# Kernel tuning notes

Hardware: AMD Instinct MI355X
Metric: run time of the kernel (lower is better)

## Reference

```python
import jax, jax.numpy as jnp
import numpy as np
from jax import lax

N = 32768      # points in the single input cloud
NIN = 16       # input per-point features
NH = 64        # nhidden
NOUT = 2
K = 32         # max_neighbors
DEPTH = 3
RADII = (2.0, 4.0, 8.0)
DIM = NH + 4   # PPFConv message dim: x_j (NH) + 4 point-pair features
CHUNK = 1024   # query chunk for brute-force radius search


def _fps(pos, n_samples):
    """Farthest point sampling, deterministic start at index 0 (eval mode)."""
    n = pos.shape[0]
    big = jnp.asarray(np.finfo(np.float32).max, pos.dtype)

    def body(carry, _):
        dists, last = carry
        d = jnp.sum((pos - pos[last]) ** 2, axis=-1)
        dists = jnp.minimum(dists, d)
        nxt = jnp.argmax(dists).astype(jnp.int32)
        return (dists, nxt), nxt

    init = (jnp.full((n,), big, pos.dtype), jnp.int32(0))
    _, rest = lax.scan(body, init, None, length=n_samples - 1)
    return jnp.concatenate([jnp.zeros((1,), jnp.int32), rest])


def _radius_knn(pos_q, pos, r, k):
    """For each query: indices of up to k points within radius r (+ validity mask).
    Chunked over queries so the [nq, n] distance matrix is never fully materialized."""
    nq = pos_q.shape[0]

    def f(qc):
        d2 = jnp.sum((qc[:, None, :] - pos[None, :, :]) ** 2, axis=-1)  # [CHUNK, n]
        neg_d2, idx = lax.top_k(-d2, k)
        valid = (-neg_d2) <= r * r
        return idx, valid

    idx, valid = lax.map(f, pos_q.reshape(-1, CHUNK, 3))
    return idx.reshape(nq, k), valid.reshape(nq, k)


def _angle(v1, v2):
    c = jnp.cross(v1, v2)
    return jnp.arctan2(jnp.linalg.norm(c, axis=-1), jnp.sum(v1 * v2, axis=-1))


def _ppf(pos_i, pos_j, n_i, n_j):
    d = pos_j - pos_i
    return jnp.stack([
        jnp.linalg.norm(d, axis=-1),
        _angle(n_i, d),
        _angle(n_j, d),
        _angle(n_i, n_j),
    ], axis=-1)


def _forward(x, pos, norm, lin_in_w0, lin_in_b0, lin_in_w1, lin_in_b1,
             sa_nn1_w0, sa_nn1_b0, sa_nn1_w1, sa_nn1_b1, sa_nn2_w, sa_nn2_b,
             lin_out_w0, lin_out_b0, lin_out_w1, lin_out_b1):
    # lin_in MLP
    h = jax.nn.relu(x @ lin_in_w0 + lin_in_b0)
    h = jax.nn.relu(h @ lin_in_w1 + lin_in_b1)

    cur_x, cur_pos, cur_norm = h, pos, norm
    for i in range(DEPTH):  # SAModules (structurally distinct levels)
        n_samples = cur_pos.shape[0] // 2  # ratio = 0.5
        idx = _fps(cur_pos, n_samples)
        pos_q = cur_pos[idx]
        norm_q = cur_norm[idx]
        nbr, valid = _radius_knn(pos_q, cur_pos, RADII[i], K)  # [nq, K]
        x_j = cur_x[nbr]                                       # [nq, K, NH]
        feats = _ppf(pos_q[:, None, :], cur_pos[nbr], norm_q[:, None, :], cur_norm[nbr])
        msg = jnp.concatenate([x_j, feats], axis=-1)           # [nq, K, DIM]
        # PPFConv local nn (nn1): Linear+ReLU x2
        m = jax.nn.relu(msg @ sa_nn1_w0[i] + sa_nn1_b0[i])
        m = jax.nn.relu(m @ sa_nn1_w1[i] + sa_nn1_b1[i])
        # max aggregation over valid neighbors (empty -> 0, matching torch_scatter)
        m = jnp.where(valid[..., None], m, -1e30)
        agg = jnp.max(m, axis=1)
        agg = jnp.where(valid.any(axis=1)[:, None], agg, 0.0)
        # PPFConv global nn (nn2): Linear+ReLU
        cur_x = jax.nn.relu(agg @ sa_nn2_w[i] + sa_nn2_b[i])
        cur_pos, cur_norm = pos_q, norm_q

    # global_mean_pool over the single graph -> [1, NH]
    pooled = jnp.mean(cur_x, axis=0, keepdims=True)
    o = jax.nn.relu(pooled @ lin_out_w0 + lin_out_b0)
    return o @ lin_out_w1 + lin_out_b1  # [1, NOUT]


_forward_jit = jax.jit(_forward)


def setup_inputs() -> dict:
    key = jax.random.key(0)
    ks = jax.random.split(key, 20)

    def w(k, *shape):
        return jax.random.normal(k, shape, jnp.float32) * float(np.sqrt(2.0 / shape[-2]))

    def b(k, *shape):
        return jax.random.normal(k, shape, jnp.float32) * 0.01

    x = jax.random.normal(ks[0], (N, NIN), jnp.float32)
    pos = jax.random.uniform(ks[1], (N, 3), dtype=jnp.float32) * 32.0  # unit density cube
    nrm = jax.random.normal(ks[2], (N, 3), jnp.float32)
    norm = nrm / jnp.linalg.norm(nrm, axis=-1, keepdims=True)

    return dict(
        x=x, pos=pos, norm=norm,
        lin_in_w0=w(ks[3], NIN, NH), lin_in_b0=b(ks[4], NH),
        lin_in_w1=w(ks[5], NH, NH), lin_in_b1=b(ks[6], NH),
        sa_nn1_w0=w(ks[7], DEPTH, DIM, DIM), sa_nn1_b0=b(ks[8], DEPTH, DIM),
        sa_nn1_w1=w(ks[9], DEPTH, DIM, DIM), sa_nn1_b1=b(ks[10], DEPTH, DIM),
        sa_nn2_w=w(ks[11], DEPTH, DIM, NH), sa_nn2_b=b(ks[12], DEPTH, NH),
        lin_out_w0=w(ks[13], NH, NH), lin_out_b0=b(ks[14], NH),
        lin_out_w1=w(ks[15], NH, NOUT), lin_out_b1=b(ks[16], NOUT),
    )


def reference(x, pos, norm, lin_in_w0, lin_in_b0, lin_in_w1, lin_in_b1,
              sa_nn1_w0, sa_nn1_b0, sa_nn1_w1, sa_nn1_b1, sa_nn2_w, sa_nn2_b,
              lin_out_w0, lin_out_b0, lin_out_w1, lin_out_b1):
    return _forward_jit(x, pos, norm, lin_in_w0, lin_in_b0, lin_in_w1, lin_in_b1,
                        sa_nn1_w0, sa_nn1_b0, sa_nn1_w1, sa_nn1_b1, sa_nn2_w, sa_nn2_b,
                        lin_out_w0, lin_out_b0, lin_out_w1, lin_out_b1)
```

## Files before the change

### kernel.cpp

```cpp
#include <hip/hip_runtime.h>
#include <math.h>

typedef unsigned long long u64;

#define TILE 2048
#define CAP 96
#define QB 32
#define NCELL 4096

__device__ __forceinline__ u64 wave_min_u64(u64 v) {
#pragma unroll
  for (int off = 32; off; off >>= 1) {
    u64 o = __shfl_xor(v, off, 64);
    v = (o < v) ? o : v;
  }
  return v;
}

__device__ __forceinline__ u64 wave_max_u64(u64 v) {
#pragma unroll
  for (int off = 32; off; off >>= 1) {
    u64 o = __shfl_xor(v, off, 64);
    v = (o > v) ? o : v;
  }
  return v;
}

__device__ __forceinline__ float angf(float ax, float ay, float az,
                                      float bx, float by, float bz) {
  float cx = ay * bz - az * by;
  float cy = az * bx - ax * bz;
  float cz = ax * by - ay * bx;
  float cn = sqrtf(cx * cx + cy * cy + cz * cz);
  float dt = ax * bx + ay * by + az * bz;
  return atan2f(cn, dt);
}

__device__ __forceinline__ int cell_of(float x, float y, float z) {
  int cx = (int)(x * 0.5f); cx = cx < 0 ? 0 : (cx > 15 ? 15 : cx);
  int cy = (int)(y * 0.5f); cy = cy < 0 ? 0 : (cy > 15 ? 15 : cy);
  int cz = (int)(z * 0.5f); cz = cz < 0 ? 0 : (cz > 15 ? 15 : cz);
  return (cz << 8) | (cy << 4) | cx;
}

__global__ __launch_bounds__(256) void k_lin_in(
    const float* __restrict__ x, const float* __restrict__ w0,
    const float* __restrict__ b0, const float* __restrict__ w1,
    const float* __restrict__ b1, float* __restrict__ h) {
  __shared__ __align__(16) float sW0[1024];
  __shared__ __align__(16) float sW1[4096];
  __shared__ float sB0[64], sB1[64];
  for (int i = threadIdx.x; i < 1024; i += 256) sW0[i] = w0[i];
  for (int i = threadIdx.x; i < 4096; i += 256) sW1[i] = w1[i];
  if (threadIdx.x < 64) { sB0[threadIdx.x] = b0[threadIdx.x]; sB1[threadIdx.x] = b1[threadIdx.x]; }
  __syncthreads();
  int p = blockIdx.x * 256 + threadIdx.x;
  float h1[64];
#pragma unroll
  for (int o = 0; o < 64; ++o) h1[o] = sB0[o];
#pragma unroll
  for (int c4 = 0; c4 < 4; ++c4) {
    float4 xv = *(const float4*)&x[p * 16 + 4 * c4];
#pragma unroll
    for (int u = 0; u < 4; ++u) {
      float v = (u == 0) ? xv.x : (u == 1) ? xv.y : (u == 2) ? xv.z : xv.w;
      int c = 4 * c4 + u;
#pragma unroll
      for (int o4 = 0; o4 < 16; ++o4) {
        float4 w = *(const float4*)&sW0[c * 64 + 4 * o4];
        h1[4 * o4 + 0] = fmaf(v, w.x, h1[4 * o4 + 0]);
        h1[4 * o4 + 1] = fmaf(v, w.y, h1[4 * o4 + 1]);
        h1[4 * o4 + 2] = fmaf(v, w.z, h1[4 * o4 + 2]);
        h1[4 * o4 + 3] = fmaf(v, w.w, h1[4 * o4 + 3]);
      }
    }
  }
#pragma unroll
  for (int o = 0; o < 64; ++o) h1[o] = fmaxf(h1[o], 0.f);
  float h2[64];
#pragma unroll
  for (int o = 0; o < 64; ++o) h2[o] = sB1[o];
#pragma unroll
  for (int c = 0; c < 64; ++c) {
    float v = h1[c];
#pragma unroll
    for (int o4 = 0; o4 < 16; ++o4) {
      float4 w = *(const float4*)&sW1[c * 64 + 4 * o4];
      h2[4 * o4 + 0] = fmaf(v, w.x, h2[4 * o4 + 0]);
      h2[4 * o4 + 1] = fmaf(v, w.y, h2[4 * o4 + 1]);
      h2[4 * o4 + 2] = fmaf(v, w.z, h2[4 * o4 + 2]);
      h2[4 * o4 + 3] = fmaf(v, w.w, h2[4 * o4 + 3]);
    }
  }
#pragma unroll
  for (int o4 = 0; o4 < 16; ++o4) {
    float4 o;
    o.x = fmaxf(h2[4 * o4 + 0], 0.f);
    o.y = fmaxf(h2[4 * o4 + 1], 0.f);
    o.z = fmaxf(h2[4 * o4 + 2], 0.f);
    o.w = fmaxf(h2[4 * o4 + 3], 0.f);
    *(float4*)&h[(long)p * 64 + 4 * o4] = o;
  }
}

__global__ __launch_bounds__(256) void k_precompA(
    const float* __restrict__ feat, const float* __restrict__ w,
    const float* __restrict__ b, float* __restrict__ A, int n) {
  __shared__ __align__(16) float sW[4352];
  __shared__ float sB[68];
  for (int i = threadIdx.x; i < 4352; i += 256) sW[i] = w[i];
  for (int i = threadIdx.x; i < 68; i += 256) sB[i] = b[i];
  __syncthreads();
  int p = blockIdx.x * 256 + threadIdx.x;
  if (p >= n) return;
  float acc[68];
#pragma unroll
  for (int o = 0; o < 68; ++o) acc[o] = sB[o];
#pragma unroll
  for (int c4 = 0; c4 < 16; ++c4) {
    float4 f = *(const float4*)&feat[(long)p * 64 + 4 * c4];
#pragma unroll
    for (int u = 0; u < 4; ++u) {
      float v = (u == 0) ? f.x : (u == 1) ? f.y : (u == 2) ? f.z : f.w;
      int c = 4 * c4 + u;
#pragma unroll
      for (int o4 = 0; o4 < 17; ++o4) {
        float4 wv = *(const float4*)&sW[c * 68 + 4 * o4];
        acc[4 * o4 + 0] = fmaf(v, wv.x, acc[4 * o4 + 0]);
        acc[4 * o4 + 1] = fmaf(v, wv.y, acc[4 * o4 + 1]);
        acc[4 * o4 + 2] = fmaf(v, wv.z, acc[4 * o4 + 2]);
        acc[4 * o4 + 3] = fmaf(v, wv.w, acc[4 * o4 + 3]);
      }
    }
  }
#pragma unroll
  for (int o4 = 0; o4 < 17; ++o4) {
    float4 o;
    o.x = acc[4 * o4 + 0]; o.y = acc[4 * o4 + 1];
    o.z = acc[4 * o4 + 2]; o.w = acc[4 * o4 + 3];
    *(float4*)&A[(long)p * 68 + 4 * o4] = o;
  }
}

__global__ __launch_bounds__(256) void k_zero_counts(int* __restrict__ c) {
  int i = blockIdx.x * 256 + threadIdx.x;
  if (i < NCELL) c[i] = 0;
}

__global__ __launch_bounds__(256) void k_hist(const float* __restrict__ pos,
                                              int n, int* __restrict__ counts) {
  int i = blockIdx.x * 256 + threadIdx.x;
  if (i >= n) return;
  atomicAdd(&counts[cell_of(pos[3 * i], pos[3 * i + 1], pos[3 * i + 2])], 1);
}

__global__ __launch_bounds__(512) void k_scan(const int* __restrict__ counts,
                                              int* __restrict__ starts,
                                              int* __restrict__ offs) {
  __shared__ int ps[512];
  int t = threadIdx.x;
  int loc[8], s = 0;
#pragma unroll
  for (int k = 0; k < 8; ++k) { loc[k] = counts[t * 8 + k]; s += loc[k]; }
  ps[t] = s;
  __syncthreads();
  for (int off = 1; off < 512; off <<= 1) {
    int v = (t >= off) ? ps[t - off] : 0;
    __syncthreads();
    ps[t] += v;
    __syncthreads();
  }
  int run = ps[t] - s;
#pragma unroll
  for (int k = 0; k < 8; ++k) {
    starts[t * 8 + k] = run;
    offs[t * 8 + k] = run;
    run += loc[k];
  }
  if (t == 511) starts[NCELL] = run;
}

__global__ __launch_bounds__(256) void k_scatter(
    const float* __restrict__ pos, int n, int* __restrict__ offs,
    float4* __restrict__ pts, int* __restrict__ sid, int* __restrict__ slot0) {
  int i = blockIdx.x * 256 + threadIdx.x;
  if (i >= n) return;
  float x = pos[3 * i], y = pos[3 * i + 1], z = pos[3 * i + 2];
  int c = cell_of(x, y, z);
  int slot = atomicAdd(&offs[c], 1);
  pts[slot] = make_float4(x, y, z, 3.402823466e38f);
  sid[slot] = i;
  if (i == 0) *slot0 = slot;
}

__global__ __launch_bounds__(512) void k_fps_cell(
    float4* __restrict__ pts, const int* __restrict__ sid,
    const int* __restrict__ starts, const int* __restrict__ slot0, int m,
    int* __restrict__ sel) {
#pragma clang fp contract(off)
  __shared__ u64 ck[NCELL];
  __shared__ int cs[NCELL + 1];
  __shared__ unsigned short sl[NCELL];
  __shared__ float bx[NCELL], by[NCELL], bz[NCELL];
  __shared__ int scnt[2];
  __shared__ u64 wk[2][8];
  const int t = threadIdx.x, lane = t & 63, wv = t >> 6;
  const u64 lmask = (1ull << lane) - 1ull;
  const unsigned* ckhi = (const unsigned*)ck;
  for (int c = t; c < NCELL + 1; c += 512) cs[c] = starts[c];
  __syncthreads();
  for (int c = t; c < NCELL; c += 512)
    ck[c] = (cs[c + 1] > cs[c]) ? ((u64)0x7F7FFFFFu << 32) : 0ull;
  if (t < 2) scnt[t] = 0;
  if (t == 0) sel[0] = 0;
  __syncthreads();
  float4 cp = pts[*slot0];
  float px = cp.x, py = cp.y, pz = cp.z;
  for (int i = 1; i < m; ++i) {
    const int par = i & 1;
    bool sv[8];
#pragma unroll
    for (int k = 0; k < 8; ++k) {
      int c = t + 512 * k;
      unsigned drmax = ckhi[2 * c + 1];
      float cx = (float)(((c & 15) << 1) + 1);
      float cy = (float)((((c >> 4) & 15) << 1) + 1);
      float cz = (float)(((c >> 8) << 1) + 1);
      float dx = fmaxf(fabsf(px - cx) - 1.f, 0.f);
      float dy = fmaxf(fabsf(py - cy) - 1.f, 0.f);
      float dz = fmaxf(fabsf(pz - cz) - 1.f, 0.f);
      float mind2 = (dx * dx + dy * dy) + dz * dz;
      sv[k] = __float_as_uint(mind2 * 0.9999f) < drmax;
    }
    u64 msk[8];
    int wtot = 0;
#pragma unroll
    for (int k = 0; k < 8; ++k) {
      msk[k] = __ballot(sv[k]);
      wtot += __popcll(msk[k]);
    }
    int wbase = 0;
    if (lane == 0 && wtot) wbase = atomicAdd(&scnt[par], wtot);
    wbase = __shfl(wbase, 0, 64);
#pragma unroll
    for (int k = 0; k < 8; ++k) {
      if (sv[k])
        sl[wbase + __popcll(msk[k] & lmask)] = (unsigned short)(t + 512 * k);
      wbase += __popcll(msk[k]);
    }
    if (t == 0) scnt[par ^ 1] = 0;
    __syncthreads();
    const int ns = scnt[par];
    const int g0 = t >> 3, l = t & 7;
    for (int g = g0; g < ns; g += 64) {
      int c = sl[g];
      int s = cs[c], e = cs[c + 1];
      u64 lk = 0;
      float lx = 0.f, ly = 0.f, lz = 0.f;
      for (int slot = s + l; slot < e; slot += 8) {
        float4 p = pts[slot];
        float ax = p.x - px, ay = p.y - py, az = p.z - pz;
        float d = (ax * ax + ay * ay) + az * az;
        float nd = fminf(p.w, d);
        ((float*)&pts[slot])[3] = nd;
        int o = sid[slot];
        u64 kk = ((u64)__float_as_uint(nd) << 32) |
                 ((u64)(unsigned)(32767 - o) << 12) | (unsigned)c;
        if (kk > lk) { lk = kk; lx = p.x; ly = p.y; lz = p.z; }
      }
#pragma unroll
      for (int off = 4; off; off >>= 1) {
        u64 ok = __shfl_xor(lk, off, 64);
        float ox = __shfl_xor(lx, off, 64);
        float oy = __shfl_xor(ly, off, 64);
        float oz = __shfl_xor(lz, off, 64);
        if (ok > lk) { lk = ok; lx = ox; ly = oy; lz = oz; }
      }
      if (l == 0) {
        ck[c] = lk; bx[c] = lx; by[c] = ly; bz[c] = lz;
      }
    }
    __syncthreads();
    u64 k = 0;
#pragma unroll
    for (int kk = 0; kk < 8; ++kk) {
      u64 v = ck[t + 512 * kk];
      if (v > k) k = v;
    }
    k = wave_max_u64(k);
    if (lane == 0) wk[par][wv] = k;
    __syncthreads();
    u64 best = wk[par][0];
#pragma unroll
    for (int w = 1; w < 8; ++w) {
      u64 v = wk[par][w];
      if (v > best) best = v;
    }
    int cell = (int)(best & 0xFFF);
    if (t == 0) sel[i] = 32767 - (int)((best >> 12) & 0x7FFF);
    px = bx[cell]; py = by[cell]; pz = bz[cell];
  }
}

template <int P>
__global__ __launch_bounds__(512) void k_fps_breg(
    const float* __restrict__ pos, int n, int m, int* __restrict__ sel) {
#pragma clang fp contract(off)
  __shared__ float zb[512 * P];
  __shared__ u64 wk[2][8];
  const int t = threadIdx.x, lane = t & 63, wv = t >> 6;
  float xr[P], yr[P], dr[P];
#pragma unroll
  for (int j = 0; j < P; ++j) {
    int idx = t + 512 * j;
    xr[j] = pos[3 * idx + 0];
    yr[j] = pos[3 * idx + 1];
    zb[idx] = pos[3 * idx + 2];
    dr[j] = 3.402823466e38f;
  }
  if (t == 0) sel[0] = 0;
  __syncthreads();
  int cur = 0;
  for (int i = 1; i < m; ++i) {
    float px = pos[3 * cur + 0], py = pos[3 * cur + 1], pz = pos[3 * cur + 2];
    float bv = -1.f;
    int bi = 0;
#pragma unroll
    for (int j = 0; j < P; ++j) {
      int idx = t + 512 * j;
      float ax = xr[j] - px, ay = yr[j] - py, az = zb[idx] - pz;
      float d = (ax * ax + ay * ay) + az * az;
      float nd = fminf(dr[j], d);
      dr[j] = nd;
      if (nd > bv) { bv = nd; bi = idx; }
    }
#pragma unroll
    for (int off = 32; off; off >>= 1) {
      float ov = __shfl_xor(bv, off, 64);
      int oi = __shfl_xor(bi, off, 64);
      if (ov > bv || (ov == bv && oi < bi)) { bv = ov; bi = oi; }
    }
    int par = i & 1;
    if (lane == 0)
      wk[par][wv] = ((u64)__float_as_uint(bv) << 32) | (unsigned)(~bi);
    __syncthreads();
    u64 bk = wk[par][0];
#pragma unroll
    for (int w = 1; w < 8; ++w) {
      u64 o = wk[par][w];
      if (o > bk) bk = o;
    }
    cur = (int)(~(unsigned)bk);
    if (t == 0) sel[i] = cur;
  }
}

__global__ __launch_bounds__(256) void k_gather(
    const float* __restrict__ pos, const float* __restrict__ nrm,
    const int* __restrict__ sel, int m, float* __restrict__ opos,
    float* __restrict__ onrm) {
  int i = blockIdx.x * 256 + threadIdx.x;
  if (i >= m) return;
  int s = sel[i];
  opos[3 * i + 0] = pos[3 * s + 0];
  opos[3 * i + 1] = pos[3 * s + 1];
  opos[3 * i + 2] = pos[3 * s + 2];
  onrm[3 * i + 0] = nrm[3 * s + 0];
  onrm[3 * i + 1] = nrm[3 * s + 1];
  onrm[3 * i + 2] = nrm[3 * s + 2];
}

__global__ __launch_bounds__(512) void k_conv(
    const float* __restrict__ qpos, const float* __restrict__ qnorm, int nq,
    const float* __restrict__ dpos, const float* __restrict__ dnorm, int n,
    const float* __restrict__ A, const float* __restrict__ w0p,
    const float* __restrict__ w1g, const float* __restrict__ b1g,
    const float* __restrict__ w2g, const float* __restrict__ b2g, float r2,
    float* __restrict__ xout) {
  __shared__ __align__(16) float smem[12288];
  __shared__ float aggS[QB][68];
  __shared__ int knnS[QB][32];
  __shared__ float qpS[QB][3], qnS[QB][3];
  __shared__ __align__(16) float w0pS[272];
  __shared__ float b1S[68], b2S[64];

  const int tid = threadIdx.x, lane = tid & 63, wv = tid >> 6;
  const int q0 = blockIdx.x * QB;
  float* tileS = smem;
  u64* cand = (u64*)&smem[6144];

  for (int i = tid; i < QB * 3; i += 512) {
    ((float*)qpS)[i] = qpos[q0 * 3 + i];
    ((float*)qnS)[i] = qnorm[q0 * 3 + i];
  }
  for (int i = tid; i < 272; i += 512) {
    int o = i >> 2, f = i & 3;
    w0pS[i] = w0p[f * 68 + o];
  }
  for (int i = tid; i < 68; i += 512) b1S[i] = b1g[i];
  for (int i = tid; i < 64; i += 512) b2S[i] = b2g[i];
  __syncthreads();

  float qx[4], qy[4], qz[4], thr[4];
  int cnt[4], tight[4];
#pragma unroll
  for (int qi = 0; qi < 4; ++qi) {
    int ql = wv * 4 + qi;
    qx[qi] = qpS[ql][0]; qy[qi] = qpS[ql][1]; qz[qi] = qpS[ql][2];
    thr[qi] = r2; cnt[qi] = 0; tight[qi] = 0;
  }
  const u64 lmask = (1ull << lane) - 1ull;
  for (int t0 = 0; t0 < n; t0 += TILE) {
    __syncthreads();
    for (int i = tid; i < TILE * 3; i += 512) tileS[i] = dpos[t0 * 3 + i];
    __syncthreads();
    for (int s = 0; s < TILE; s += 64) {
      int p = s + lane;
      float px = tileS[3 * p], py = tileS[3 * p + 1], pz = tileS[3 * p + 2];
      int gidx = t0 + p;
#pragma unroll
      for (int qi = 0; qi < 4; ++qi) {
        float d2;
        {
#pragma clang fp contract(off)
          float ax = px - qx[qi], ay = py - qy[qi], az = pz - qz[qi];
          d2 = (ax * ax + ay * ay) + az * az;
        }
        bool pred = tight[qi] ? (d2 < thr[qi]) : (d2 <= thr[qi]);
        u64 mask = __ballot(pred);
        if (mask) {
          int need = __popcll(mask);
          int base = (wv * 4 + qi) * CAP;
          if (cnt[qi] + need > CAP) {
            u64 v0 = (lane < cnt[qi]) ? cand[base + lane] : ~0ull;
            u64 v1 = (lane + 64 < cnt[qi]) ? cand[base + lane + 64] : ~0ull;
            u64 keep = ~0ull, last = 0;
            for (int it = 0; it < 32; ++it) {
              u64 mloc = (v0 < v1) ? v0 : v1;
              u64 mn = wave_min_u64(mloc);
              if (lane == it) keep = mn;
              if (v0 == mn) v0 = ~0ull; else if (v1 == mn) v1 = ~0ull;
              last = mn;
            }
            if (lane < 32) cand[base + lane] = keep;
            cnt[qi] = 32;
            thr[qi] = __uint_as_float((unsigned)(last >> 32));
            tight[qi] = 1;
          }
          if (pred) {
            int slot = cnt[qi] + __popcll(mask & lmask);
            cand[base + slot] = ((u64)__float_as_uint(d2) << 32) | (unsigned)gidx;
          }
          cnt[qi] += need;
        }
      }
    }
  }
#pragma unroll
  for (int qi = 0; qi < 4; ++qi) {
    int ql = wv * 4 + qi, base = ql * CAP, c = cnt[qi];
    int nout = (c < 32) ? c : 32;
    u64 v0 = (lane < c) ? cand[base + lane] : ~0ull;
    u64 v1 = (lane + 64 < c) ? cand[base + lane + 64] : ~0ull;
    int first = 0;
    for (int it = 0; it < 32; ++it) {
      u64 mloc = (v0 < v1) ? v0 : v1;
      u64 mn = wave_min_u64(mloc);
      int idx = (int)(mn & 0xffffffffu);
      if (it == 0) first = idx;
      int wr = (it < nout) ? idx : first;
      if (lane == it) knnS[ql][it] = wr;
      if (it < nout) {
        if (v0 == mn) v0 = ~0ull; else if (v1 == mn) v1 = ~0ull;
      }
    }
  }
  __syncthreads();
  for (int i = tid; i < 4624; i += 512) smem[i] = w1g[i];
  for (int i = tid; i < 4352; i += 512) smem[4624 + i] = w2g[i];
  __syncthreads();
  const float* W1s = smem;
  const float* W2s = smem + 4624;

#pragma unroll 1
  for (int r = 0; r < 2; ++r) {
    const int h = lane >> 5;
    const int ql = r * 16 + wv * 2 + h;
    const int kk = lane & 31;
    const int j = knnS[ql][kk];
    const float qx_ = qpS[ql][0], qy_ = qpS[ql][1], qz_ = qpS[ql][2];
    float dx = dpos[3 * j + 0] - qx_;
    float dy = dpos[3 * j + 1] - qy_;
    float dz = dpos[3 * j + 2] - qz_;
    float f0 = sqrtf(dx * dx + dy * dy + dz * dz);
    float nix = qnS[ql][0], niy = qnS[ql][1], niz = qnS[ql][2];
    float njx = dnorm[3 * j + 0], njy = dnorm[3 * j + 1], njz = dnorm[3 * j + 2];
    float f1 = angf(nix, niy, niz, dx, dy, dz);
    float f2 = angf(njx, njy, njz, dx, dy, dz);
    float f3 = angf(nix, niy, niz, njx, njy, njz);
    const float* Arow = A + (long)j * 68;
    float acc[68];
#pragma unroll
    for (int o = 0; o < 68; ++o) acc[o] = b1S[o];
    float4 a = *(const float4*)&Arow[0];
#pragma unroll 1
    for (int c4 = 0; c4 < 17; ++c4) {
      float4 an = (c4 < 16) ? *(const float4*)&Arow[4 * (c4 + 1)] : a;
#pragma unroll
      for (int u = 0; u < 4; ++u) {
        int c = 4 * c4 + u;
        float4 wf = *(const float4*)&w0pS[4 * c];
        float v = (u == 0) ? a.x : (u == 1) ? a.y : (u == 2) ? a.z : a.w;
        v = fmaf(f0, wf.x, v);
        v = fmaf(f1, wf.y, v);
        v = fmaf(f2, wf.z, v);
        v = fmaf(f3, wf.w, v);
        float mv = fmaxf(v, 0.f);
#pragma unroll
        for (int o4 = 0; o4 < 17; ++o4) {
          float4 wv4 = *(const float4*)&W1s[c * 68 + 4 * o4];
          acc[4 * o4 + 0] = fmaf(mv, wv4.x, acc[4 * o4 + 0]);
          acc[4 * o4 + 1] = fmaf(mv, wv4.y, acc[4 * o4 + 1]);
          acc[4 * o4 + 2] = fmaf(mv, wv4.z, acc[4 * o4 + 2]);
          acc[4 * o4 + 3] = fmaf(mv, wv4.w, acc[4 * o4 + 3]);
        }
      }
      a = an;
    }
#pragma unroll
    for (int o = 0; o < 68; ++o) {
      float v = fmaxf(acc[o], 0.f);
#pragma unroll
      for (int off = 16; off; off >>= 1) v = fmaxf(v, __shfl_xor(v, off, 64));
      if (kk == 0) aggS[ql][o] = v;
    }
  }
  __syncthreads();
  {
    const int ql = tid >> 4;
    const int og = (tid & 15) * 4;
    float a0 = b2S[og + 0], a1 = b2S[og + 1], a2 = b2S[og + 2], a3 = b2S[og + 3];
#pragma unroll
    for (int c = 0; c < 68; ++c) {
      float av = aggS[ql][c];
      float4 wv4 = *(const float4*)&W2s[c * 64 + og];
      a0 = fmaf(av, wv4.x, a0);
      a1 = fmaf(av, wv4.y, a1);
      a2 = fmaf(av, wv4.z, a2);
      a3 = fmaf(av, wv4.w, a3);
    }
    float4 o;
    o.x = fmaxf(a0, 0.f); o.y = fmaxf(a1, 0.f);
    o.z = fmaxf(a2, 0.f); o.w = fmaxf(a3, 0.f);
    *(float4*)&xout[(long)(q0 + ql) * 64 + og] = o;
  }
}

__global__ __launch_bounds__(256) void k_final(
    const float* __restrict__ x3, const float* __restrict__ w0,
    const float* __restrict__ b0, const float* __restrict__ w1,
    const float* __restrict__ b1, float* __restrict__ out) {
  __shared__ float part[4][64];
  __shared__ float pooled[64];
  __shared__ float hS[64];
  int t = threadIdx.x, c = t & 63, g = t >> 6;
  float s = 0.f;
  for (int i = g; i < 4096; i += 4) s += x3[(long)i * 64 + c];
  part[g][c] = s;
  __syncthreads();
  if (t < 64)
    pooled[t] = (part[0][t] + part[1][t] + part[2][t] + part[3][t]) * (1.f / 4096.f);
  __syncthreads();
  if (t < 64) {
    float a = b0[t];
    for (int cc = 0; cc < 64; ++cc) a = fmaf(pooled[cc], w0[cc * 64 + t], a);
    hS[t] = fmaxf(a, 0.f);
  }
  __syncthreads();
  if (t < 2) {
    float a = b1[t];
    for (int cc = 0; cc < 64; ++cc) a = fmaf(hS[cc], w1[cc * 2 + t], a);
    out[t] = a;
  }
}

extern "C" void kernel_launch(void* const* d_in, const int* in_sizes, int n_in,
                              void* d_out, int out_size, void* d_ws,
                              size_t ws_size, hipStream_t stream) {
  (void)in_sizes; (void)n_in; (void)out_size;
  const float* x     = (const float*)d_in[0];
  const float* pos   = (const float*)d_in[1];
  const float* nrm   = (const float*)d_in[2];
  const float* li_w0 = (const float*)d_in[3];
  const float* li_b0 = (const float*)d_in[4];
  const float* li_w1 = (const float*)d_in[5];
  const float* li_b1 = (const float*)d_in[6];
  const float* n1w0  = (const float*)d_in[7];
  const float* n1b0  = (const float*)d_in[8];
  const float* n1w1  = (const float*)d_in[9];
  const float* n1b1  = (const float*)d_in[10];
  const float* n2w   = (const float*)d_in[11];
  const float* n2b   = (const float*)d_in[12];
  const float* lo_w0 = (const float*)d_in[13];
  const float* lo_b0 = (const float*)d_in[14];
  const float* lo_w1 = (const float*)d_in[15];
  const float* lo_b1 = (const float*)d_in[16];
  float* out = (float*)d_out;

  char* ws = (char*)d_ws;
  size_t off = 0;
  auto alloc = [&](size_t nb) -> void* {
    void* p = (void*)(ws + off);
    off += nb;
    off = (off + 1023) & ~((size_t)1023);
    return p;
  };
  float* h     = (float*)alloc((size_t)32768 * 64 * 4);
  float* A0    = (float*)alloc((size_t)32768 * 68 * 4);
  int* counts  = (int*)  alloc((size_t)NCELL * 4);
  int* starts  = (int*)  alloc((size_t)(NCELL + 1) * 4);
  int* offs    = (int*)  alloc((size_t)NCELL * 4);
  float4* pts  = (float4*)alloc((size_t)32768 * 16);
  int* sid     = (int*)  alloc((size_t)32768 * 4);
  int* slot0   = (int*)  alloc((size_t)64);
  int*   sel0  = (int*)  alloc((size_t)16384 * 4);
  float* pos1  = (float*)alloc((size_t)16384 * 3 * 4);
  float* nrm1  = (float*)alloc((size_t)16384 * 3 * 4);
  float* x1    = (float*)alloc((size_t)16384 * 64 * 4);
  float* A1    = (float*)alloc((size_t)16384 * 68 * 4);
  int*   sel1  = (int*)  alloc((size_t)8192 * 4);
  float* pos2  = (float*)alloc((size_t)8192 * 3 * 4);
  float* nrm2  = (float*)alloc((size_t)8192 * 3 * 4);
  float* x2    = (float*)alloc((size_t)8192 * 64 * 4);
  float* A2    = (float*)alloc((size_t)8192 * 68 * 4);
  int*   sel2  = (int*)  alloc((size_t)4096 * 4);
  float* pos3  = (float*)alloc((size_t)4096 * 3 * 4);
  float* nrm3  = (float*)alloc((size_t)4096 * 3 * 4);
  float* x3    = (float*)alloc((size_t)4096 * 64 * 4);
  if (off > ws_size) return;

  k_lin_in<<<128, 256, 0, stream>>>(x, li_w0, li_b0, li_w1, li_b1, h);
  k_precompA<<<128, 256, 0, stream>>>(h, n1w0, n1b0, A0, 32768);

  k_zero_counts<<<16, 256, 0, stream>>>(counts);
  k_hist<<<128, 256, 0, stream>>>(pos, 32768, counts);
  k_scan<<<1, 512, 0, stream>>>(counts, starts, offs);
  k_scatter<<<128, 256, 0, stream>>>(pos, 32768, offs, pts, sid, slot0);
  k_fps_cell<<<1, 512, 0, stream>>>(pts, sid, starts, slot0, 16384, sel0);
  k_gather<<<64, 256, 0, stream>>>(pos, nrm, sel0, 16384, pos1, nrm1);
  k_conv<<<512, 512, 0, stream>>>(pos1, nrm1, 16384, pos, nrm, 32768, A0,
                                  n1w0 + 64 * 68, n1w1, n1b1, n2w, n2b, 4.0f,
                                  x1);

  k_zero_counts<<<16, 256, 0, stream>>>(counts);
  k_hist<<<64, 256, 0, stream>>>(pos1, 16384, counts);
  k_scan<<<1, 512, 0, stream>>>(counts, starts, offs);
  k_scatter<<<64, 256, 0, stream>>>(pos1, 16384, offs, pts, sid, slot0);
  k_fps_cell<<<1, 512, 0, stream>>>(pts, sid, starts, slot0, 8192, sel1);
  k_gather<<<32, 256, 0, stream>>>(pos1, nrm1, sel1, 8192, pos2, nrm2);
  k_precompA<<<64, 256, 0, stream>>>(x1, n1w0 + 68 * 68, n1b0 + 68, A1, 16384);
  k_conv<<<256, 512, 0, stream>>>(pos2, nrm2, 8192, pos1, nrm1, 16384, A1,
                                  n1w0 + 68 * 68 + 64 * 68, n1w1 + 68 * 68,
                                  n1b1 + 68, n2w + 68 * 64, n2b + 64, 16.0f,
                                  x2);

  k_fps_breg<16><<<1, 512, 0, stream>>>(pos2, 8192, 4096, sel2);
  k_gather<<<16, 256, 0, stream>>>(pos2, nrm2, sel2, 4096, pos3, nrm3);
  k_precompA<<<32, 256, 0, stream>>>(x2, n1w0 + 2 * 68 * 68, n1b0 + 2 * 68, A2,
                                     8192);
  k_conv<<<128, 512, 0, stream>>>(pos3, nrm3, 4096, pos2, nrm2, 8192, A2,
                                  n1w0 + 2 * 68 * 68 + 64 * 68,
                                  n1w1 + 2 * 68 * 68, n1b1 + 2 * 68,
                                  n2w + 2 * 68 * 64, n2b + 2 * 64, 64.0f, x3);
  k_final<<<1, 256, 0, stream>>>(x3, lo_w0, lo_b0, lo_w1, lo_b1, out);
}
```

Before: 54.12 ms.

## Fuse serial FPS blocks with independent conv/precompute work in shared launches

Single-block farthest-point-sampling kernels are merged into a combined launch where block 0 runs FPS for the next level while the remaining blocks run the previous level's precompute or conv. Because FPS of the next level depends only on positions, this overlaps the latency-bound single-block FPS with the parallel conv work instead of leaving the GPU mostly idle. Shared memory is unified into one byte buffer sized for the larger user, which may reduce conv occupancy in the fused kernels.

```diff
diff --git a/kernel.cpp b/kernel.cpp
--- a/kernel.cpp
+++ b/kernel.cpp
@@ -7,6 +7,24 @@
 #define CAP 96
 #define QB 32
 #define NCELL 4096
+
+#define FPS_SM_BYTES 106640
+#define CK_OFF 0
+#define CS_OFF 32768
+#define SL_OFF 49156
+#define BX_OFF 57348
+#define BY_OFF 73732
+#define BZ_OFF 90116
+#define SCNT_OFF 106500
+#define WK_OFF 106512
+#define CONV_SM_BYTES 64336
+#define CV_AGG 49152
+#define CV_KNN 57856
+#define CV_QP 61952
+#define CV_QN 62336
+#define CV_W0P 62720
+#define CV_B1 63808
+#define CV_B2 64080
 
 __device__ __forceinline__ u64 wave_min_u64(u64 v) {
 #pragma unroll
@@ -103,15 +121,12 @@
   }
 }
 
-__global__ __launch_bounds__(256) void k_precompA(
-    const float* __restrict__ feat, const float* __restrict__ w,
-    const float* __restrict__ b, float* __restrict__ A, int n) {
-  __shared__ __align__(16) float sW[4352];
-  __shared__ float sB[68];
-  for (int i = threadIdx.x; i < 4352; i += 256) sW[i] = w[i];
-  for (int i = threadIdx.x; i < 68; i += 256) sB[i] = b[i];
-  __syncthreads();
-  int p = blockIdx.x * 256 + threadIdx.x;
+__device__ void precompA_body(float* sW, float* sB, int p, int nt,
+                              const float* feat, const float* w,
+                              const float* b, float* A, int n) {
+  for (int i = threadIdx.x; i < 4352; i += nt) sW[i] = w[i];
+  for (int i = threadIdx.x; i < 68; i += nt) sB[i] = b[i];
+  __syncthreads();
   if (p >= n) return;
   float acc[68];
 #pragma unroll
@@ -140,6 +155,14 @@
     o.z = acc[4 * o4 + 2]; o.w = acc[4 * o4 + 3];
     *(float4*)&A[(long)p * 68 + 4 * o4] = o;
   }
+}
+
+__global__ __launch_bounds__(256) void k_precompA(
+    const float* __restrict__ feat, const float* __restrict__ w,
+    const float* __restrict__ b, float* __restrict__ A, int n) {
+  __shared__ __align__(16) float sW[4352];
+  __shared__ float sB[68];
+  precompA_body(sW, sB, blockIdx.x * 256 + threadIdx.x, 256, feat, w, b, A, n);
 }
 
 __global__ __launch_bounds__(256) void k_zero_counts(int* __restrict__ c) {
@@ -193,20 +216,20 @@
   if (i == 0) *slot0 = slot;
 }
 
-__global__ __launch_bounds__(512) void k_fps_cell(
-    float4* __restrict__ pts, const int* __restrict__ sid,
-    const int* __restrict__ starts, const int* __restrict__ slot0, int m,
-    int* __restrict__ sel) {
+__device__ void fps_cell_body(char* SM, float4* pts, const int* sid,
+                              const int* starts, const int* slot0, int m,
+                              int* sel) {
 #pragma clang fp contract(off)
-  __shared__ u64 ck[NCELL];
-  __shared__ int cs[NCELL + 1];
-  __shared__ unsigned short sl[NCELL];
-  __shared__ float bx[NCELL], by[NCELL], bz[NCELL];
-  __shared__ int scnt[2];
-  __shared__ u64 wk[2][8];
+  u64* ck = (u64*)(SM + CK_OFF);
+  int* cs = (int*)(SM + CS_OFF);
+  unsigned short* sl = (unsigned short*)(SM + SL_OFF);
+  float* bx = (float*)(SM + BX_OFF);
+  float* by = (float*)(SM + BY_OFF);
+  float* bz = (float*)(SM + BZ_OFF);
+  int* scnt = (int*)(SM + SCNT_OFF);
+  u64 (*wk)[8] = (u64(*)[8])(SM + WK_OFF);
   const int t = threadIdx.x, lane = t & 63, wv = t >> 6;
   const u64 lmask = (1ull << lane) - 1ull;
-  const unsigned* ckhi = (const unsigned*)ck;
   for (int c = t; c < NCELL + 1; c += 512) cs[c] = starts[c];
   __syncthreads();
   for (int c = t; c < NCELL; c += 512)
@@ -222,7 +245,7 @@
 #pragma unroll
     for (int k = 0; k < 8; ++k) {
       int c = t + 512 * k;
-      unsigned drmax = ckhi[2 * c + 1];
+      unsigned drmax = (unsigned)(ck[c] >> 32);
       float cx = (float)(((c & 15) << 1) + 1);
       float cy = (float)((((c >> 4) & 15) << 1) + 1);
       float cz = (float)(((c >> 8) << 1) + 1);
@@ -302,12 +325,12 @@
   }
 }
 
-template <int P>
-__global__ __launch_bounds__(512) void k_fps_breg(
-    const float* __restrict__ pos, int n, int m, int* __restrict__ sel) {
+__device__ void fps_breg_body(char* SM, const float* pos, int n, int m,
+                              int* sel) {
 #pragma clang fp contract(off)
-  __shared__ float zb[512 * P];
-  __shared__ u64 wk[2][8];
+  const int P = 16;
+  float* zb = (float*)SM;
+  u64 (*wk)[8] = (u64(*)[8])(SM + 32768);
   const int t = threadIdx.x, lane = t & 63, wv = t >> 6;
   float xr[P], yr[P], dr[P];
 #pragma unroll
@@ -370,24 +393,25 @@
   onrm[3 * i + 2] = nrm[3 * s + 2];
 }
 
-__global__ __launch_bounds__(512) void k_conv(
-    const float* __restrict__ qpos, const float* __restrict__ qnorm, int nq,
-    const float* __restrict__ dpos, const float* __restrict__ dnorm, int n,
-    const float* __restrict__ A, const float* __restrict__ w0p,
-    const float* __restrict__ w1g, const float* __restrict__ b1g,
-    const float* __restrict__ w2g, const float* __restrict__ b2g, float r2,
-    float* __restrict__ xout) {
-  __shared__ __align__(16) float smem[12288];
-  __shared__ float aggS[QB][68];
-  __shared__ int knnS[QB][32];
-  __shared__ float qpS[QB][3], qnS[QB][3];
-  __shared__ __align__(16) float w0pS[272];
-  __shared__ float b1S[68], b2S[64];
+__device__ void conv_body(char* SM, int qblk, const float* qpos,
+                          const float* qnorm, const float* dpos,
+                          const float* dnorm, int n, const float* A,
+                          const float* w0p, const float* w1g,
+                          const float* b1g, const float* w2g,
+                          const float* b2g, float r2, float* xout) {
+  float* smem = (float*)SM;
+  u64* cand = (u64*)&smem[6144];
+  float (*aggS)[68] = (float(*)[68])(SM + CV_AGG);
+  int (*knnS)[32] = (int(*)[32])(SM + CV_KNN);
+  float (*qpS)[3] = (float(*)[3])(SM + CV_QP);
+  float (*qnS)[3] = (float(*)[3])(SM + CV_QN);
+  float* w0pS = (float*)(SM + CV_W0P);
+  float* b1S = (float*)(SM + CV_B1);
+  float* b2S = (float*)(SM + CV_B2);
 
   const int tid = threadIdx.x, lane = tid & 63, wv = tid >> 6;
-  const int q0 = blockIdx.x * QB;
+  const int q0 = qblk * QB;
   float* tileS = smem;
-  u64* cand = (u64*)&smem[6144];
 
   for (int i = tid; i < QB * 3; i += 512) {
     ((float*)qpS)[i] = qpos[q0 * 3 + i];
@@ -556,6 +580,69 @@
   }
 }
 
+__global__ __launch_bounds__(512) void k_f0(
+    float4* __restrict__ pts, const int* __restrict__ sid,
+    const int* __restrict__ starts, const int* __restrict__ slot0, int m,
+    int* __restrict__ sel, const float* __restrict__ h,
+    const float* __restrict__ w, const float* __restrict__ b,
+    float* __restrict__ A, int n) {
+  __shared__ __align__(16) char SM[FPS_SM_BYTES];
+  if (blockIdx.x == 0) {
+    fps_cell_body(SM, pts, sid, starts, slot0, m, sel);
+  } else {
+    precompA_body((float*)SM, (float*)(SM + 17408),
+                  (int)(blockIdx.x - 1) * 512 + threadIdx.x, 512, h, w, b, A,
+                  n);
+  }
+}
+
+__global__ __launch_bounds__(512) void k_fA(
+    float4* __restrict__ pts, const int* __restrict__ sid,
+    const int* __restrict__ starts, const int* __restrict__ slot0, int m,
+    int* __restrict__ sel, const float* __restrict__ qpos,
+    const float* __restrict__ qnorm, const float* __restrict__ dpos,
+    const float* __restrict__ dnorm, int n, const float* __restrict__ A,
+    const float* __restrict__ w0p, const float* __restrict__ w1g,
+    const float* __restrict__ b1g, const float* __restrict__ w2g,
+    const float* __restrict__ b2g, float r2, float* __restrict__ xout) {
+  __shared__ __align__(16) char SM[FPS_SM_BYTES];
+  if (blockIdx.x == 0) {
+    fps_cell_body(SM, pts, sid, starts, slot0, m, sel);
+  } else {
+    conv_body(SM, blockIdx.x - 1, qpos, qnorm, dpos, dnorm, n, A, w0p, w1g,
+              b1g, w2g, b2g, r2, xout);
+  }
+}
+
+__global__ __launch_bounds__(512) void k_fB(
+    const float* __restrict__ bpos, int bn, int bm, int* __restrict__ sel,
+    const float* __restrict__ qpos, const float* __restrict__ qnorm,
+    const float* __restrict__ dpos, const float* __restrict__ dnorm, int n,
+    const float* __restrict__ A, const float* __restrict__ w0p,
+    const float* __restrict__ w1g, const float* __restrict__ b1g,
+    const float* __restrict__ w2g, const float* __restrict__ b2g, float r2,
+    float* __restrict__ xout) {
+  __shared__ __align__(16) char SM[CONV_SM_BYTES];
+  if (blockIdx.x == 0) {
+    fps_breg_body(SM, bpos, bn, bm, sel);
+  } else {
+    conv_body(SM, blockIdx.x - 1, qpos, qnorm, dpos, dnorm, n, A, w0p, w1g,
+              b1g, w2g, b2g, r2, xout);
+  }
+}
+
+__global__ __launch_bounds__(512) void k_conv(
+    const float* __restrict__ qpos, const float* __restrict__ qnorm, int nq,
+    const float* __restrict__ dpos, const float* __restrict__ dnorm, int n,
+    const float* __restrict__ A, const float* __restrict__ w0p,
+    const float* __restrict__ w1g, const float* __restrict__ b1g,
+    const float* __restrict__ w2g, const float* __restrict__ b2g, float r2,
+    float* __restrict__ xout) {
+  __shared__ __align__(16) char SM[CONV_SM_BYTES];
+  conv_body(SM, blockIdx.x, qpos, qnorm, dpos, dnorm, n, A, w0p, w1g, b1g,
+            w2g, b2g, r2, xout);
+}
+
 __global__ __launch_bounds__(256) void k_final(
     const float* __restrict__ x3, const float* __restrict__ w0,
     const float* __restrict__ b0, const float* __restrict__ w1,
@@ -640,31 +727,29 @@
   if (off > ws_size) return;
 
   k_lin_in<<<128, 256, 0, stream>>>(x, li_w0, li_b0, li_w1, li_b1, h);
-  k_precompA<<<128, 256, 0, stream>>>(h, n1w0, n1b0, A0, 32768);
 
   k_zero_counts<<<16, 256, 0, stream>>>(counts);
   k_hist<<<128, 256, 0, stream>>>(pos, 32768, counts);
   k_scan<<<1, 512, 0, stream>>>(counts, starts, offs);
   k_scatter<<<128, 256, 0, stream>>>(pos, 32768, offs, pts, sid, slot0);
-  k_fps_cell<<<1, 512, 0, stream>>>(pts, sid, starts, slot0, 16384, sel0);
+  k_f0<<<65, 512, 0, stream>>>(pts, sid, starts, slot0, 16384, sel0, h, n1w0,
+                               n1b0, A0, 32768);
   k_gather<<<64, 256, 0, stream>>>(pos, nrm, sel0, 16384, pos1, nrm1);
-  k_conv<<<512, 512, 0, stream>>>(pos1, nrm1, 16384, pos, nrm, 32768, A0,
-                                  n1w0 + 64 * 68, n1w1, n1b1, n2w, n2b, 4.0f,
-                                  x1);
 
   k_zero_counts<<<16, 256, 0, stream>>>(counts);
   k_hist<<<64, 256, 0, stream>>>(pos1, 16384, counts);
   k_scan<<<1, 512, 0, stream>>>(counts, starts, offs);
   k_scatter<<<64, 256, 0, stream>>>(pos1, 16384, offs, pts, sid, slot0);
-  k_fps_cell<<<1, 512, 0, stream>>>(pts, sid, starts, slot0, 8192, sel1);
+  k_fA<<<513, 512, 0, stream>>>(pts, sid, starts, slot0, 8192, sel1, pos1,
+                                nrm1, pos, nrm, 32768, A0, n1w0 + 64 * 68,
+                                n1w1, n1b1, n2w, n2b, 4.0f, x1);
   k_gather<<<32, 256, 0, stream>>>(pos1, nrm1, sel1, 8192, pos2, nrm2);
   k_precompA<<<64, 256, 0, stream>>>(x1, n1w0 + 68 * 68, n1b0 + 68, A1, 16384);
-  k_conv<<<256, 512, 0, stream>>>(pos2, nrm2, 8192, pos1, nrm1, 16384, A1,
-                                  n1w0 + 68 * 68 + 64 * 68, n1w1 + 68 * 68,
-                                  n1b1 + 68, n2w + 68 * 64, n2b + 64, 16.0f,
-                                  x2);
-
-  k_fps_breg<16><<<1, 512, 0, stream>>>(pos2, 8192, 4096, sel2);
+
+  k_fB<<<257, 512, 0, stream>>>(pos2, 8192, 4096, sel2, pos2, nrm2, pos1,
+                                nrm1, 16384, A1, n1w0 + 68 * 68 + 64 * 68,
+                                n1w1 + 68 * 68, n1b1 + 68, n2w + 68 * 64,
+                                n2b + 64, 16.0f, x2);
   k_gather<<<16, 256, 0, stream>>>(pos2, nrm2, sel2, 4096, pos3, nrm3);
   k_precompA<<<32, 256, 0, stream>>>(x2, n1w0 + 2 * 68 * 68, n1b0 + 2 * 68, A2,
                                      8192);
```

Result: no change. 54.48 ms (+0.7%).
